# Performance work log

Measured on AMD Instinct MI355X. Metric: run time of the kernel, lower is better.

## Reference

```python
import jax, jax.numpy as jnp
import numpy as np


def setup_inputs() -> dict:
    key = jax.random.key(0)
    ks = jax.random.split(key, 8)
    B, C, W, H = 4, 256, 64, 64
    Cq = C // 8
    return {
        "input": jax.random.normal(ks[0], (B, C, W, H), dtype=jnp.float32),
        "Wf": jax.random.normal(ks[1], (Cq, C), dtype=jnp.float32) * 0.05,
        "bf": jax.random.normal(ks[2], (Cq,), dtype=jnp.float32) * 0.05,
        "Wg": jax.random.normal(ks[3], (Cq, C), dtype=jnp.float32) * 0.05,
        "bg": jax.random.normal(ks[4], (Cq,), dtype=jnp.float32) * 0.05,
        "Wh": jax.random.normal(ks[5], (C, C), dtype=jnp.float32) * 0.05,
        "bh": jax.random.normal(ks[6], (C,), dtype=jnp.float32) * 0.05,
        "gamma": jax.random.normal(ks[7], (1,), dtype=jnp.float32),
    }


def reference(input, Wf, bf, Wg, bg, Wh, bh, gamma):
    # input: [B, C, W, H]; SAGAN self-attention over N = W*H spatial tokens.
    B, C, W, H = input.shape
    N = W * H
    x = input.reshape(B, C, N)
    # 1x1 Conv1d == per-token linear projection over channels.
    f = jnp.einsum('oc,bcn->bon', Wf, x) + bf[None, :, None]  # [B, C/8, N]
    g = jnp.einsum('oc,bcn->bon', Wg, x) + bg[None, :, None]  # [B, C/8, N]
    h = jnp.einsum('oc,bcn->bon', Wh, x) + bh[None, :, None]  # [B, C,   N]
    # s = f^T g -> [B, N, N]; softmax over last dim (columns / g-tokens).
    s = jnp.einsum('bon,bom->bnm', f, g)
    attention = jax.nn.softmax(s, axis=-1)
    # out = h @ attention^T : out[b,c,m] = sum_n h[b,c,n] * attention[b,m,n]
    out = jnp.einsum('bcn,bmn->bcm', h, attention)
    out = out.reshape(B, C, W, H)
    return gamma[0] * out + input
```

## Files before the change

### kernel.cpp

```cpp
#include <hip/hip_runtime.h>

typedef _Float16 half8 __attribute__((ext_vector_type(8)));
typedef _Float16 half4 __attribute__((ext_vector_type(4)));
typedef float floatx16 __attribute__((ext_vector_type(16)));

#define MFMA_F16(A, B, C) __builtin_amdgcn_mfma_f32_32x32x16_f16(A, B, C, 0, 0, 0)

constexpr int Bn = 4;
constexpr int Cc = 256;
constexpr int Cq = 32;
constexpr int Nn = 4096;
constexpr float LOG2E = 1.44269504088896340736f;


__device__ inline floatx16 zero16() {
  floatx16 z;
#pragma unroll
  for (int i = 0; i < 16; ++i) z[i] = 0.f;
  return z;
}

__global__ __launch_bounds__(256) void k_wconv(
    const float* __restrict__ Wf, const float* __restrict__ Wg,
    const float* __restrict__ Wh, _Float16* __restrict__ Wfh,
    _Float16* __restrict__ Wgh, _Float16* __restrict__ Whh) {
  int e = (blockIdx.x * 256 + threadIdx.x) * 4;
  const float* src;
  _Float16* dst;
  float sc = 1.f;
  if (e < 8192) { src = Wf + e; dst = Wfh + e; sc = LOG2E; }
  else if (e < 16384) { src = Wg + (e - 8192); dst = Wgh + (e - 8192); }
  else { src = Wh + (e - 16384); dst = Whh + (e - 16384); }
  float4 v = *(const float4*)src;
  half4 o;
  o[0] = (_Float16)(v.x * sc); o[1] = (_Float16)(v.y * sc);
  o[2] = (_Float16)(v.z * sc); o[3] = (_Float16)(v.w * sc);
  *(half4*)dst = o;
}

__global__ __launch_bounds__(256) void k_proj(
    const float* __restrict__ x,
    const _Float16* __restrict__ Wfh, const float* __restrict__ bf,
    const _Float16* __restrict__ Wgh, const float* __restrict__ bg,
    const _Float16* __restrict__ Whh, const float* __restrict__ bh,
    _Float16* __restrict__ Q, _Float16* __restrict__ K4,
    _Float16* __restrict__ V8) {
  int tid = threadIdx.x;
  int w = tid >> 6, lane = tid & 63;
  int ml = lane & 31, h = lane >> 5;
  int b = blockIdx.x >> 7, nt = blockIdx.x & 127;
  int n0 = nt * 32;
  const float* xb = x + (size_t)b * Cc * Nn + n0 + ml;

  for (int t = w; t < 10; t += 4) {
    const _Float16* W;
    const float* bias;
    float bscale = 1.f;
    int o0 = 0;
    if (t == 0) { W = Wfh; bias = bf; bscale = LOG2E; }
    else if (t == 1) { W = Wgh; bias = bg; }
    else { W = Whh + (size_t)(t - 2) * 32 * Cc; bias = bh + (t - 2) * 32; o0 = (t - 2) * 32; }

    floatx16 acc = zero16();
    const _Float16* wp = W + (size_t)ml * Cc + h * 8;
#pragma unroll
    for (int kc = 0; kc < 16; ++kc) {
      half8 a = *(const half8*)(wp + kc * 16);
      const float* xp = xb + (size_t)(kc * 16 + h * 8) * Nn;
      half8 bfr;
#pragma unroll
      for (int j = 0; j < 8; ++j) bfr[j] = (_Float16)xp[(size_t)j * Nn];
      acc = MFMA_F16(a, bfr, acc);
    }

    if (t == 0) {
      _Float16* op = Q + ((size_t)b * Nn + n0 + ml) * Cq;
#pragma unroll
      for (int qd = 0; qd < 4; ++qd) {
        float4 bq = *(const float4*)(bias + 8 * qd + 4 * h);
        const float* bqp = (const float*)&bq;
#pragma unroll
        for (int i = 0; i < 4; ++i) {
          int crow = i + 8 * qd + 4 * h;
          op[crow] = (_Float16)(acc[4 * qd + i] + bqp[i] * bscale);
        }
      }
    } else if (t == 1) {
#pragma unroll
      for (int qd = 0; qd < 4; ++qd) {
        float4 bq = *(const float4*)(bias + 8 * qd + 4 * h);
        const float* bqp = (const float*)&bq;
#pragma unroll
        for (int i = 0; i < 4; ++i) {
          int crow = i + 8 * qd + 4 * h;
          K4[(((size_t)b * 4 + (crow >> 3)) * Nn + n0 + ml) * 8 + (crow & 7)] =
              (_Float16)(acc[4 * qd + i] + bqp[i]);
        }
      }
    } else {
      size_t nb = (size_t)((n0 + ml) >> 3);
      _Float16* op = V8 + (((size_t)b * 512 + nb) * 256) * 8 + (ml & 7);
#pragma unroll
      for (int qd = 0; qd < 4; ++qd) {
        float4 bq = *(const float4*)(bias + 8 * qd + 4 * h);
        const float* bqp = (const float*)&bq;
#pragma unroll
        for (int i = 0; i < 4; ++i) {
          int crow = i + 8 * qd + 4 * h;
          op[(size_t)(o0 + crow) * 8] = (_Float16)(acc[4 * qd + i] + bqp[i]);
        }
      }
    }
  }
}

__global__ __launch_bounds__(512) void k_rowmax(const _Float16* __restrict__ Q,
                                                const _Float16* __restrict__ K4,
                                                float* __restrict__ M) {
  __shared__ float red[8][32];
  int tid = threadIdx.x, w = tid >> 6, lane = tid & 63;
  int ml = lane & 31, h = lane >> 5;
  int b = blockIdx.x >> 7, mt = blockIdx.x & 127;
  int m0 = mt * 32;
  const _Float16* qp = Q + ((size_t)b * Nn + m0 + ml) * Cq + h * 8;
  half8 qb0 = *(const half8*)(qp);
  half8 qb1 = *(const half8*)(qp + 16);
  const _Float16* kp0 = K4 + (((size_t)b * 4 + h) * Nn + w * 512 + ml) * 8;
  const _Float16* kp1 = K4 + (((size_t)b * 4 + 2 + h) * Nn + w * 512 + ml) * 8;
  float mx = -3.0e38f;
  for (int t = 0; t < 16; ++t) {
    floatx16 s = zero16();
    half8 k0 = *(const half8*)(kp0 + (size_t)t * 32 * 8);
    half8 k1 = *(const half8*)(kp1 + (size_t)t * 32 * 8);
    s = MFMA_F16(k0, qb0, s);
    s = MFMA_F16(k1, qb1, s);
#pragma unroll
    for (int i = 0; i < 16; ++i) mx = fmaxf(mx, s[i]);
  }
  mx = fmaxf(mx, __shfl_xor(mx, 32, 64));
  if (h == 0) red[w][ml] = mx;
  __syncthreads();
  if (tid < 32) {
    float m2 = red[0][tid];
#pragma unroll
    for (int i = 1; i < 8; ++i) m2 = fmaxf(m2, red[i][tid]);
    M[(size_t)b * Nn + m0 + tid] = m2;
  }
}

__global__ __launch_bounds__(512, 4) void k_attn(
    const _Float16* __restrict__ Q, const _Float16* __restrict__ K4,
    const _Float16* __restrict__ V8, const float* __restrict__ M,
    _Float16* __restrict__ Opart, float* __restrict__ lpart, int nspan) {
  __shared__ _Float16 P[2 * 64 * 128];
  __shared__ float lred[8][32];
  int tid = threadIdx.x, w = tid >> 6, lane = tid & 63;
  int ml = lane & 31, h = lane >> 5;
  int msub = w & 1, nq = w >> 1;
  int bx = blockIdx.x;
  int mt = bx & 63, b = (bx >> 6) & 3, nc = bx >> 8;
  int m0 = mt * 64;
  int nbase0 = nc * nspan;
  int sw = ml & 15;

  const _Float16* qp = Q + ((size_t)b * Nn + m0 + msub * 32 + ml) * Cq + h * 8;
  half8 qb0 = *(const half8*)(qp);
  half8 qb1 = *(const half8*)(qp + 16);
  float Mv = M[(size_t)b * Nn + m0 + msub * 32 + ml];
  float lacc = 0.f;

  const _Float16* k4b0 =
      K4 + (((size_t)b * 4 + h) * Nn + nbase0 + nq * 32 + ml) * 8;
  const _Float16* k4b1 =
      K4 + (((size_t)b * 4 + 2 + h) * Nn + nbase0 + nq * 32 + ml) * 8;

  int c0 = w * 32;
  const _Float16* v8b =
      V8 + (((size_t)b * 512 + (nbase0 >> 3)) * 256 + c0 + ml) * 8;

  floatx16 o0 = zero16(), o1 = zero16();
  int iters = nspan >> 7;
  _Float16* pwbase = &P[(msub * 32 + ml) * 128];
  const _Float16* pr0 = &P[ml * 128];
  const _Float16* pr1 = &P[(32 + ml) * 128];

  for (int it = 0; it < iters; ++it) {
    int bufo = (it & 1) * (64 * 128);
    {
      floatx16 s = zero16();
      half8 k0 = *(const half8*)(k4b0 + (size_t)it * 128 * 8);
      half8 k1 = *(const half8*)(k4b1 + (size_t)it * 128 * 8);
      s = MFMA_F16(k0, qb0, s);
      s = MFMA_F16(k1, qb1, s);
      _Float16* pw = pwbase + bufo;
#pragma unroll
      for (int q = 0; q < 4; ++q) {
        float p0 = exp2f(s[4 * q + 0] - Mv);
        float p1 = exp2f(s[4 * q + 1] - Mv);
        float p2 = exp2f(s[4 * q + 2] - Mv);
        float p3 = exp2f(s[4 * q + 3] - Mv);
        lacc += (p0 + p1) + (p2 + p3);
        half4 pk;
        pk[0] = (_Float16)p0; pk[1] = (_Float16)p1;
        pk[2] = (_Float16)p2; pk[3] = (_Float16)p3;
        *(half4*)(pw + ((nq * 4 + q) ^ sw) * 8 + 4 * h) = pk;
      }
    }
    __syncthreads();
    {
      const _Float16* vp = v8b + (size_t)it * 16 * 2048;
      const _Float16* p0b = pr0 + bufo;
      const _Float16* p1b = pr1 + bufo;
#pragma unroll
      for (int kc = 0; kc < 8; ++kc) {
        half8 vf = *(const half8*)(vp + (size_t)(kc * 2 + h) * 2048);
        int chunk = (kc * 2 + h) ^ sw;
        half8 pb0 = *(const half8*)(p0b + chunk * 8);
        half8 pb1 = *(const half8*)(p1b + chunk * 8);
        o0 = MFMA_F16(vf, pb0, o0);
        o1 = MFMA_F16(vf, pb1, o1);
      }
    }
  }

  lacc += __shfl_xor(lacc, 32, 64);
  if (h == 0) lred[w][ml] = lacc;
  __syncthreads();
  if (w < 2 && h == 0) {
    float lsum = lred[w][ml] + lred[w + 2][ml] + lred[w + 4][ml] + lred[w + 6][ml];
    lpart[((size_t)nc * Bn + b) * Nn + m0 + w * 32 + ml] = lsum;
  }

  _Float16* op0 = Opart + ((size_t)((size_t)nc * Bn + b) * Cc) * Nn + (m0 + ml);
#pragma unroll
  for (int r = 0; r < 16; ++r) {
    int c = c0 + (r & 3) + 8 * (r >> 2) + 4 * h;
    op0[(size_t)c * Nn] = (_Float16)o0[r];
    op0[(size_t)c * Nn + 32] = (_Float16)o1[r];
  }
}

__global__ __launch_bounds__(256) void k_fin(const _Float16* __restrict__ Op,
                                             const float* __restrict__ lp,
                                             const float* __restrict__ inp,
                                             const float* __restrict__ gamma,
                                             float* __restrict__ out, int NC) {
  int i4 = (blockIdx.x * 256 + threadIdx.x) * 4;
  int m = i4 & (Nn - 1);
  int bc = i4 >> 12;
  int b = bc >> 8;
  float ax = 0.f, ay = 0.f, az = 0.f, aw = 0.f;
  float lx = 0.f, ly = 0.f, lz = 0.f, lw = 0.f;
  for (int nc = 0; nc < NC; ++nc) {
    half4 o = *(const half4*)(Op + ((size_t)nc * Bn * Cc + bc) * Nn + m);
    float4 lv = *(const float4*)(lp + ((size_t)nc * Bn + b) * Nn + m);
    ax += (float)o[0]; ay += (float)o[1]; az += (float)o[2]; aw += (float)o[3];
    lx += lv.x; ly += lv.y; lz += lv.z; lw += lv.w;
  }
  float g = gamma[0];
  float4 xi = *(const float4*)(inp + (size_t)i4);
  float4 r;
  r.x = g * ax / lx + xi.x;
  r.y = g * ay / ly + xi.y;
  r.z = g * az / lz + xi.z;
  r.w = g * aw / lw + xi.w;
  *(float4*)(out + (size_t)i4) = r;
}

extern "C" void kernel_launch(void* const* d_in, const int* in_sizes, int n_in,
                              void* d_out, int out_size, void* d_ws,
                              size_t ws_size, hipStream_t stream) {
  const float* x = (const float*)d_in[0];
  const float* Wf = (const float*)d_in[1];
  const float* bf = (const float*)d_in[2];
  const float* Wg = (const float*)d_in[3];
  const float* bg = (const float*)d_in[4];
  const float* Wh = (const float*)d_in[5];
  const float* bh = (const float*)d_in[6];
  const float* gamma = (const float*)d_in[7];
  float* out = (float*)d_out;

  char* ws = (char*)d_ws;
  _Float16* Q  = (_Float16*)(ws);
  _Float16* K4 = (_Float16*)(ws + 1048576);
  _Float16* V8 = (_Float16*)(ws + 2097152);
  float*    M  = (float*)   (ws + 10485760);
  _Float16* Wfh = (_Float16*)(ws + 10551296);
  _Float16* Wgh = (_Float16*)(ws + 10567680);
  _Float16* Whh = (_Float16*)(ws + 10584064);
  float*    lpart = (float*)(ws + 10715136);
  _Float16* Opart = (_Float16*)(ws + 10846208);

  size_t base = 10846208u;
  int NC = (ws_size >= base + 2u * 8388608u) ? 2 : 1;
  int nspan = Nn / NC;

  k_wconv<<<dim3(80), dim3(256), 0, stream>>>(Wf, Wg, Wh, Wfh, Wgh, Whh);
  k_proj<<<dim3(512), dim3(256), 0, stream>>>(x, Wfh, bf, Wgh, bg, Whh, bh, Q, K4, V8);
  k_rowmax<<<dim3(512), dim3(512), 0, stream>>>(Q, K4, M);
  k_attn<<<dim3(NC * 256), dim3(512), 0, stream>>>(Q, K4, V8, M, Opart, lpart, nspan);
  k_fin<<<dim3(4096), dim3(256), 0, stream>>>(Opart, lpart, x, gamma, out, NC);
}
```

Before: 170.5 us.

## Pre-tile projection weights for coalesced loads and allow four-way attention key split

The weight conversion kernel now writes the fp16 weights in a tiled layout, grouped by 8-channel chunks and then output row. The projection kernel's MFMA A-fragment loads then become contiguous across lanes instead of strided by the channel count. The launcher also enlarges the partial-softmax buffer and, when the workspace is large enough, splits the attention key range four ways instead of two. That gives the attention kernel more blocks to spread across CUs, at the cost of more partial outputs for the finalize kernel to merge.

```diff
diff --git a/kernel.cpp b/kernel.cpp
--- a/kernel.cpp
+++ b/kernel.cpp
@@ -22,27 +22,41 @@
 
 __global__ __launch_bounds__(256) void k_wconv(
     const float* __restrict__ Wf, const float* __restrict__ Wg,
-    const float* __restrict__ Wh, _Float16* __restrict__ Wfh,
-    _Float16* __restrict__ Wgh, _Float16* __restrict__ Whh) {
+    const float* __restrict__ Wh, _Float16* __restrict__ Wf4,
+    _Float16* __restrict__ Wg4, _Float16* __restrict__ Wh4) {
   int e = (blockIdx.x * 256 + threadIdx.x) * 4;
   const float* src;
   _Float16* dst;
   float sc = 1.f;
-  if (e < 8192) { src = Wf + e; dst = Wfh + e; sc = LOG2E; }
-  else if (e < 16384) { src = Wg + (e - 8192); dst = Wgh + (e - 8192); }
-  else { src = Wh + (e - 16384); dst = Whh + (e - 16384); }
+  if (e < 8192) {
+    int o = e >> 8, c = e & 255;
+    src = Wf + e;
+    dst = Wf4 + (((c >> 3) * 32 + o) << 3) + (c & 7);
+    sc = LOG2E;
+  } else if (e < 16384) {
+    int e0 = e - 8192;
+    int o = e0 >> 8, c = e0 & 255;
+    src = Wg + e0;
+    dst = Wg4 + (((c >> 3) * 32 + o) << 3) + (c & 7);
+  } else {
+    int e0 = e - 16384;
+    int o = e0 >> 8, c = e0 & 255;
+    int ot = o >> 5, orr = o & 31;
+    src = Wh + e0;
+    dst = Wh4 + ot * 8192 + (((c >> 3) * 32 + orr) << 3) + (c & 7);
+  }
   float4 v = *(const float4*)src;
-  half4 o;
-  o[0] = (_Float16)(v.x * sc); o[1] = (_Float16)(v.y * sc);
-  o[2] = (_Float16)(v.z * sc); o[3] = (_Float16)(v.w * sc);
-  *(half4*)dst = o;
+  half4 o4;
+  o4[0] = (_Float16)(v.x * sc); o4[1] = (_Float16)(v.y * sc);
+  o4[2] = (_Float16)(v.z * sc); o4[3] = (_Float16)(v.w * sc);
+  *(half4*)dst = o4;
 }
 
 __global__ __launch_bounds__(256) void k_proj(
     const float* __restrict__ x,
-    const _Float16* __restrict__ Wfh, const float* __restrict__ bf,
-    const _Float16* __restrict__ Wgh, const float* __restrict__ bg,
-    const _Float16* __restrict__ Whh, const float* __restrict__ bh,
+    const _Float16* __restrict__ Wf4, const float* __restrict__ bf,
+    const _Float16* __restrict__ Wg4, const float* __restrict__ bg,
+    const _Float16* __restrict__ Wh4, const float* __restrict__ bh,
     _Float16* __restrict__ Q, _Float16* __restrict__ K4,
     _Float16* __restrict__ V8) {
   int tid = threadIdx.x;
@@ -53,19 +67,18 @@
   const float* xb = x + (size_t)b * Cc * Nn + n0 + ml;
 
   for (int t = w; t < 10; t += 4) {
-    const _Float16* W;
+    const _Float16* W4;
     const float* bias;
     float bscale = 1.f;
     int o0 = 0;
-    if (t == 0) { W = Wfh; bias = bf; bscale = LOG2E; }
-    else if (t == 1) { W = Wgh; bias = bg; }
-    else { W = Whh + (size_t)(t - 2) * 32 * Cc; bias = bh + (t - 2) * 32; o0 = (t - 2) * 32; }
+    if (t == 0) { W4 = Wf4; bias = bf; bscale = LOG2E; }
+    else if (t == 1) { W4 = Wg4; bias = bg; }
+    else { W4 = Wh4 + (size_t)(t - 2) * 8192; bias = bh + (t - 2) * 32; o0 = (t - 2) * 32; }
 
     floatx16 acc = zero16();
-    const _Float16* wp = W + (size_t)ml * Cc + h * 8;
 #pragma unroll
     for (int kc = 0; kc < 16; ++kc) {
-      half8 a = *(const half8*)(wp + kc * 16);
+      half8 a = *(const half8*)(W4 + ((((kc * 2 + h) * 32) + ml) << 3));
       const float* xp = xb + (size_t)(kc * 16 + h * 8) * Nn;
       half8 bfr;
 #pragma unroll
@@ -285,18 +298,20 @@
   _Float16* K4 = (_Float16*)(ws + 1048576);
   _Float16* V8 = (_Float16*)(ws + 2097152);
   float*    M  = (float*)   (ws + 10485760);
-  _Float16* Wfh = (_Float16*)(ws + 10551296);
-  _Float16* Wgh = (_Float16*)(ws + 10567680);
-  _Float16* Whh = (_Float16*)(ws + 10584064);
+  _Float16* Wf4 = (_Float16*)(ws + 10551296);
+  _Float16* Wg4 = (_Float16*)(ws + 10567680);
+  _Float16* Wh4 = (_Float16*)(ws + 10584064);
   float*    lpart = (float*)(ws + 10715136);
-  _Float16* Opart = (_Float16*)(ws + 10846208);
-
-  size_t base = 10846208u;
-  int NC = (ws_size >= base + 2u * 8388608u) ? 2 : 1;
+  _Float16* Opart = (_Float16*)(ws + 10977280);
+
+  size_t base = 10977280u;
+  int NC = 1;
+  if (ws_size >= base + 4u * 8388608u) NC = 4;
+  else if (ws_size >= base + 2u * 8388608u) NC = 2;
   int nspan = Nn / NC;
 
-  k_wconv<<<dim3(80), dim3(256), 0, stream>>>(Wf, Wg, Wh, Wfh, Wgh, Whh);
-  k_proj<<<dim3(512), dim3(256), 0, stream>>>(x, Wfh, bf, Wgh, bg, Whh, bh, Q, K4, V8);
+  k_wconv<<<dim3(80), dim3(256), 0, stream>>>(Wf, Wg, Wh, Wf4, Wg4, Wh4);
+  k_proj<<<dim3(512), dim3(256), 0, stream>>>(x, Wf4, bf, Wg4, bg, Wh4, bh, Q, K4, V8);
   k_rowmax<<<dim3(512), dim3(512), 0, stream>>>(Q, K4, M);
   k_attn<<<dim3(NC * 256), dim3(512), 0, stream>>>(Q, K4, V8, M, Opart, lpart, nspan);
   k_fin<<<dim3(4096), dim3(256), 0, stream>>>(Opart, lpart, x, gamma, out, NC);
```

Result: no change. 170.9 us (+0.2%).
